# Optimization experiments

Measured on AMD Instinct MI355X. Metric: run time of the kernel, lower is better.

## Reference

```python
import jax, jax.numpy as jnp
import numpy as np

D_MODEL = 384
H = 12
HEAD_DIM = D_MODEL // H
# Faithful to source: scale = (d_model // h) ** (-5)  (likely a typo for -0.5, but we match the code)
SCALE = float(HEAD_DIM) ** (-5.0)


def setup_inputs() -> dict:
    key = jax.random.key(0)
    ks = jax.random.split(key, 6)
    B, N, D = 4096, 49, D_MODEL
    x = jax.random.normal(ks[0], (B, N, D), dtype=jnp.float32)
    mask = jnp.zeros((B, 1, N, N), dtype=jnp.float32)
    s = 1.0 / np.sqrt(D)
    Wq = jax.random.normal(ks[1], (D, D), dtype=jnp.float32) * s
    Wk = jax.random.normal(ks[2], (D, D), dtype=jnp.float32) * s
    Wv = jax.random.normal(ks[3], (D, D), dtype=jnp.float32) * s
    Wp = jax.random.normal(ks[4], (D, D), dtype=jnp.float32) * s
    bq = jnp.zeros((D,), jnp.float32)
    bk = jnp.zeros((D,), jnp.float32)
    bv = jnp.zeros((D,), jnp.float32)
    bp = jnp.zeros((D,), jnp.float32)
    return {"x": x, "mask": mask, "Wq": Wq, "bq": bq, "Wk": Wk, "bk": bk,
            "Wv": Wv, "bv": bv, "Wp": Wp, "bp": bp}


def reference(x, mask, Wq, bq, Wk, bk, Wv, bv, Wp, bp):
    # x: [B, N, D] where B = batch*num_windows, N = window_size**2
    B, N, D = x.shape
    def heads(y):  # [B,N,D] -> [B,H,N,hd]
        return y.reshape(B, N, H, HEAD_DIM).transpose(0, 2, 1, 3)
    q = heads(x @ Wq + bq)
    k = heads(x @ Wk + bk)
    v = heads(x @ Wv + bv)
    scores = jnp.einsum('bhnd,bhmd->bhnm', q, k) * SCALE + mask  # mask broadcasts over heads
    w = jax.nn.softmax(scores, axis=-1)  # dropout=0 -> identity
    o = jnp.einsum('bhnm,bhmd->bhnd', w, v)
    o = o.transpose(0, 2, 1, 3).reshape(B, N, D)
    return o @ Wp + bp
```

## Files before the change

### kernel.cpp

```cpp
#include <hip/hip_runtime.h>


#define NWIN   4096
#define NTOK   49
#define DMODEL 384
#define NH     12
#define HD     32
#define XPITCH 392
#define QPITCH 40
#define VPITCH 72
#define SCALE  2.9802322387695312e-08f
#define NEGBIG -30000.0f

typedef __attribute__((ext_vector_type(8))) short short8;
typedef __attribute__((ext_vector_type(4))) short short4v;
typedef __attribute__((ext_vector_type(4))) float float4v;

__device__ __align__(16) unsigned short g_wT[4 * DMODEL * DMODEL];
__device__ int g_dt;

__device__ __forceinline__ float b2f(unsigned short h) {
  union { unsigned u; float f; } t; t.u = ((unsigned)h) << 16; return t.f;
}
__device__ __forceinline__ unsigned short f2b(float f) {
  union { float f; unsigned u; } t; t.f = f;
  return (unsigned short)((t.u + 0x7fffu + ((t.u >> 16) & 1u)) >> 16);
}

__global__ void detect_dtype(const unsigned short* __restrict__ x) {
  __shared__ int cnt;
  if (threadIdx.x == 0) cnt = 0;
  __syncthreads();
  int local = 0;
  for (int i = threadIdx.x; i < 2048; i += 256) {
    unsigned short h = x[2 * i];
    int e = (h >> 7) & 0xFF;
    if (e >= 0x6A && e <= 0x90) local++;
  }
  atomicAdd(&cnt, local);
  __syncthreads();
  if (threadIdx.x == 0) g_dt = (cnt < 1024) ? 1 : 0;
}

__global__ void prep_weights(const void* __restrict__ Wq,
                             const void* __restrict__ Wk,
                             const void* __restrict__ Wv,
                             const void* __restrict__ Wp) {
  int o = blockIdx.x * 256 + threadIdx.x;
  int e = o & 511;
  int t = o >> 9;
  int l = e >> 3, j = e & 7;
  int c = l & 15, qd = l >> 4;
  int k, col;
  const void* W;
  if (t < 864) {
    int h = t / 72, r = t - h * 72;
    int ks = r / 6, i = r - ks * 6;
    int mat = i >> 1, nt = i & 1;
    W = (mat == 0) ? Wq : (mat == 1) ? Wk : Wv;
    k = ks * 32 + qd * 8 + j;
    col = h * 32 + nt * 16 + c;
  } else {
    int tp = t - 864;
    int wv = tp / 72, r = tp - wv * 72;
    int ks = r / 6, nt = r - ks * 6;
    W = Wp;
    k = ks * 32 + qd * 8 + j;
    col = wv * 96 + nt * 16 + c;
  }
  unsigned short v;
  if (g_dt) v = f2b(((const float*)W)[k * DMODEL + col]);
  else      v = ((const unsigned short*)W)[k * DMODEL + col];
  g_wT[o] = v;
}

#define BAR() do {                                          \
    asm volatile("s_waitcnt lgkmcnt(0)" ::: "memory");      \
    __builtin_amdgcn_s_barrier();                           \
    asm volatile("" ::: "memory");                          \
  } while (0)

__global__ __launch_bounds__(256, 2)
void win_attn(const void* __restrict__ xg_,
              const void* __restrict__ maskg_,
              const void* __restrict__ bqg_,
              const void* __restrict__ bkg_,
              const void* __restrict__ bvg_,
              const void* __restrict__ bpg_,
              void* __restrict__ outg_)
{
  __shared__ __align__(16) short lds[28960];
  const int dt   = g_dt;
  const int win  = blockIdx.x;
  const int tid  = threadIdx.x;
  const int wv   = tid >> 6;
  const int lane = tid & 63;
  const int c    = lane & 15;
  const int qd   = lane >> 4;

  const unsigned short* const wlane = g_wT + lane * 8;

  short8 wb[12];
  #pragma unroll
  for (int t = 0; t < 12; ++t)
    wb[t] = *(const short8*)(wlane + t * 512);

  {
    unsigned* z = (unsigned*)&lds[19208];
    for (int i = tid; i < 4876; i += 256) z[i] = 0u;
  }

  if (dt == 0) {
    const uint4* src = (const uint4*)((const unsigned short*)xg_ + (size_t)win * (NTOK * DMODEL));
    for (int i = tid; i < (NTOK * DMODEL) / 8; i += 256) {
      int row = i / 48, col = i - row * 48;
      *(uint4*)&lds[row * XPITCH + col * 8] = src[i];
    }
  } else {
    const float4* src = (const float4*)((const float*)xg_ + (size_t)win * (NTOK * DMODEL));
    for (int i = tid; i < (NTOK * DMODEL) / 4; i += 256) {
      int row = i / 96, colq = i - row * 96;
      float4 f = src[i];
      short4v p;
      p[0] = (short)f2b(f.x); p[1] = (short)f2b(f.y);
      p[2] = (short)f2b(f.z); p[3] = (short)f2b(f.w);
      *(short4v*)&lds[row * XPITCH + colq * 4] = p;
    }
  }

  short* const sQ = lds + 19208;
  short* const sK = lds + 21168;
  short* const sV = lds + 23128;
  short* const sW = lds + 25432;

  const int arow = (wv * 16 + c < NTOK) ? (wv * 16 + c) : (NTOK - 1);

  float madd[4][4];
  #pragma unroll
  for (int r = 0; r < 4; ++r) {
    int m = wv * 16 + qd * 4 + r;
    #pragma unroll
    for (int nt = 0; nt < 4; ++nt) {
      int n = nt * 16 + c;
      float v;
      if (n < NTOK) {
        if (m < NTOK) {
          size_t off = (size_t)win * (NTOK * NTOK) + m * NTOK + n;
          v = dt ? ((const float*)maskg_)[off] : b2f(((const unsigned short*)maskg_)[off]);
        } else v = 0.f;
      } else v = NEGBIG;
      madd[r][nt] = v;
    }
  }

  BAR();

  short8 xa[12];
  #pragma unroll
  for (int ks = 0; ks < 12; ++ks)
    xa[ks] = *(const short8*)&lds[arow * XPITCH + ks * 32 + qd * 8];

  short* const sO = lds;

  const float4v z4 = {0.f, 0.f, 0.f, 0.f};

  #pragma unroll 1
  for (int h = 0; h < NH; ++h) {
    const unsigned short* const wh = wlane + h * 36864;

    float biasQ[2], biasK[2], biasV[2];
    #pragma unroll
    for (int nt = 0; nt < 2; ++nt) {
      const int col = h * 32 + nt * 16 + c;
      biasQ[nt] = dt ? ((const float*)bqg_)[col] : b2f(((const unsigned short*)bqg_)[col]);
      biasK[nt] = dt ? ((const float*)bkg_)[col] : b2f(((const unsigned short*)bkg_)[col]);
      biasV[nt] = dt ? ((const float*)bvg_)[col] : b2f(((const unsigned short*)bvg_)[col]);
    }

    float4v aQ0 = z4, aQ1 = z4, aK0 = z4, aK1 = z4, aV0 = z4, aV1 = z4;
    #pragma unroll
    for (int ks = 0; ks < 12; ++ks) {
      const int s = (ks & 1) * 6;
      const unsigned short* pf = (ks < 10) ? (wh + ((ks + 2) * 6) * 512)
                                           : (wh + 36864 + ((ks - 10) * 6) * 512);
      aQ0 = __builtin_amdgcn_mfma_f32_16x16x32_bf16(xa[ks], wb[s + 0], aQ0, 0, 0, 0);
      wb[s + 0] = *(const short8*)(pf + 0 * 512);
      aQ1 = __builtin_amdgcn_mfma_f32_16x16x32_bf16(xa[ks], wb[s + 1], aQ1, 0, 0, 0);
      wb[s + 1] = *(const short8*)(pf + 1 * 512);
      aK0 = __builtin_amdgcn_mfma_f32_16x16x32_bf16(xa[ks], wb[s + 2], aK0, 0, 0, 0);
      wb[s + 2] = *(const short8*)(pf + 2 * 512);
      aK1 = __builtin_amdgcn_mfma_f32_16x16x32_bf16(xa[ks], wb[s + 3], aK1, 0, 0, 0);
      wb[s + 3] = *(const short8*)(pf + 3 * 512);
      aV0 = __builtin_amdgcn_mfma_f32_16x16x32_bf16(xa[ks], wb[s + 4], aV0, 0, 0, 0);
      wb[s + 4] = *(const short8*)(pf + 4 * 512);
      aV1 = __builtin_amdgcn_mfma_f32_16x16x32_bf16(xa[ks], wb[s + 5], aV1, 0, 0, 0);
      wb[s + 5] = *(const short8*)(pf + 5 * 512);
    }

    #pragma unroll
    for (int nt = 0; nt < 2; ++nt) {
      const float4v q = nt ? aQ1 : aQ0;
      const float4v k = nt ? aK1 : aK0;
      const float4v v = nt ? aV1 : aV0;
      short4v vp;
      #pragma unroll
      for (int r = 0; r < 4; ++r) {
        const int m = wv * 16 + qd * 4 + r;
        if (m < NTOK) {
          sQ[m * QPITCH + nt * 16 + c] = (short)f2b(q[r] + biasQ[nt]);
          sK[m * QPITCH + nt * 16 + c] = (short)f2b(k[r] + biasK[nt]);
        }
        vp[r] = (short)((m < NTOK) ? f2b(v[r] + biasV[nt]) : (unsigned short)0);
      }
      *(short4v*)&sV[(nt * 16 + c) * VPITCH + wv * 16 + qd * 4] = vp;
    }
    BAR();

    float4v aS[4] = {z4, z4, z4, z4};
    {
      const short8 aq = *(const short8*)&sQ[arow * QPITCH + qd * 8];
      #pragma unroll
      for (int nt = 0; nt < 4; ++nt) {
        int kr = nt * 16 + c; if (kr > NTOK - 1) kr = NTOK - 1;
        const short8 bk8 = *(const short8*)&sK[kr * QPITCH + qd * 8];
        aS[nt] = __builtin_amdgcn_mfma_f32_16x16x32_bf16(aq, bk8, aS[nt], 0, 0, 0);
      }
    }

    #pragma unroll
    for (int r = 0; r < 4; ++r) {
      float s0 = fmaf(aS[0][r], SCALE, madd[r][0]);
      float s1 = fmaf(aS[1][r], SCALE, madd[r][1]);
      float s2 = fmaf(aS[2][r], SCALE, madd[r][2]);
      float s3 = fmaf(aS[3][r], SCALE, madd[r][3]);
      float mx = fmaxf(fmaxf(s0, s1), fmaxf(s2, s3));
      mx = fmaxf(mx, __shfl_xor(mx, 1));
      mx = fmaxf(mx, __shfl_xor(mx, 2));
      mx = fmaxf(mx, __shfl_xor(mx, 4));
      mx = fmaxf(mx, __shfl_xor(mx, 8));
      float e0 = __expf(fminf(s0 - mx, 0.f));
      float e1 = __expf(fminf(s1 - mx, 0.f));
      float e2 = __expf(fminf(s2 - mx, 0.f));
      float e3 = __expf(fminf(s3 - mx, 0.f));
      float sum = e0 + e1 + e2 + e3;
      sum += __shfl_xor(sum, 1);
      sum += __shfl_xor(sum, 2);
      sum += __shfl_xor(sum, 4);
      sum += __shfl_xor(sum, 8);
      float inv = 1.0f / sum;
      int m = wv * 16 + qd * 4 + r;
      if (m < NTOK) {
        sW[m * VPITCH +  0 + c] = (short)f2b(e0 * inv);
        sW[m * VPITCH + 16 + c] = (short)f2b(e1 * inv);
        sW[m * VPITCH + 32 + c] = (short)f2b(e2 * inv);
        sW[m * VPITCH + 48 + c] = (short)f2b(e3 * inv);
      }
    }

    float4v aO0 = z4, aO1 = z4;
    #pragma unroll
    for (int ks = 0; ks < 2; ++ks) {
      const short8 aw = *(const short8*)&sW[arow * VPITCH + ks * 32 + qd * 8];
      const short8 b0 = *(const short8*)&sV[(0 * 16 + c) * VPITCH + ks * 32 + qd * 8];
      const short8 b1 = *(const short8*)&sV[(1 * 16 + c) * VPITCH + ks * 32 + qd * 8];
      aO0 = __builtin_amdgcn_mfma_f32_16x16x32_bf16(aw, b0, aO0, 0, 0, 0);
      aO1 = __builtin_amdgcn_mfma_f32_16x16x32_bf16(aw, b1, aO1, 0, 0, 0);
    }

    #pragma unroll
    for (int r = 0; r < 4; ++r) {
      const int m = wv * 16 + qd * 4 + r;
      if (m < NTOK) {
        sO[m * XPITCH + h * 32 +  0 + c] = (short)f2b(aO0[r]);
        sO[m * XPITCH + h * 32 + 16 + c] = (short)f2b(aO1[r]);
      }
    }
    BAR();
  }

  const unsigned short* const wp = g_wT + 442368 + wv * 36864 + lane * 8;
  #pragma unroll
  for (int t = 0; t < 12; ++t)
    wb[t] = *(const short8*)(wp + t * 512);

  float biasP[6];
  #pragma unroll
  for (int nt = 0; nt < 6; ++nt) {
    const int col = wv * 96 + nt * 16 + c;
    biasP[nt] = dt ? ((const float*)bpg_)[col] : b2f(((const unsigned short*)bpg_)[col]);
  }

  float4v aP[4][6];
  #pragma unroll
  for (int mt = 0; mt < 4; ++mt)
    #pragma unroll
    for (int nt = 0; nt < 6; ++nt) aP[mt][nt] = z4;

  short8 af[2][4];
  #pragma unroll
  for (int mt = 0; mt < 4; ++mt) {
    int row = mt * 16 + c; if (row > NTOK - 1) row = NTOK - 1;
    af[0][mt] = *(const short8*)&sO[row * XPITCH + qd * 8];
  }

  #pragma unroll
  for (int ks = 0; ks < 12; ++ks) {
    const int cs = ks & 1;
    if (ks < 11) {
      #pragma unroll
      for (int mt = 0; mt < 4; ++mt) {
        int row = mt * 16 + c; if (row > NTOK - 1) row = NTOK - 1;
        af[cs ^ 1][mt] = *(const short8*)&sO[row * XPITCH + (ks + 1) * 32 + qd * 8];
      }
    }
    const int s = cs * 6;
    #pragma unroll
    for (int nt = 0; nt < 6; ++nt) {
      aP[0][nt] = __builtin_amdgcn_mfma_f32_16x16x32_bf16(af[cs][0], wb[s + nt], aP[0][nt], 0, 0, 0);
      aP[1][nt] = __builtin_amdgcn_mfma_f32_16x16x32_bf16(af[cs][1], wb[s + nt], aP[1][nt], 0, 0, 0);
      aP[2][nt] = __builtin_amdgcn_mfma_f32_16x16x32_bf16(af[cs][2], wb[s + nt], aP[2][nt], 0, 0, 0);
      aP[3][nt] = __builtin_amdgcn_mfma_f32_16x16x32_bf16(af[cs][3], wb[s + nt], aP[3][nt], 0, 0, 0);
      if (ks < 10) wb[s + nt] = *(const short8*)(wp + ((ks + 2) * 6 + nt) * 512);
    }
  }

  #pragma unroll
  for (int nt = 0; nt < 6; ++nt) {
    const int col = wv * 96 + nt * 16 + c;
    #pragma unroll
    for (int mt = 0; mt < 4; ++mt) {
      #pragma unroll
      for (int r = 0; r < 4; ++r) {
        const int m = mt * 16 + qd * 4 + r;
        if (m < NTOK) {
          const float v = aP[mt][nt][r] + biasP[nt];
          const size_t off = (size_t)win * (NTOK * DMODEL) + m * DMODEL + col;
          if (dt) ((float*)outg_)[off] = v;
          else    ((unsigned short*)outg_)[off] = f2b(v);
        }
      }
    }
  }
}

extern "C" void kernel_launch(void* const* d_in, const int* in_sizes, int n_in,
                              void* d_out, int out_size, void* d_ws, size_t ws_size,
                              hipStream_t stream) {
  const void* x    = d_in[0];
  const void* mask = d_in[1];
  const void* Wq   = d_in[2];
  const void* bq   = d_in[3];
  const void* Wk   = d_in[4];
  const void* bk   = d_in[5];
  const void* Wv   = d_in[6];
  const void* bv   = d_in[7];
  const void* Wp   = d_in[8];
  const void* bp   = d_in[9];

  detect_dtype<<<1, 256, 0, stream>>>((const unsigned short*)x);
  prep_weights<<<(4 * DMODEL * DMODEL) / 256, 256, 0, stream>>>(Wq, Wk, Wv, Wp);
  win_attn<<<NWIN, 256, 0, stream>>>(x, mask, bq, bk, bv, bp, d_out);
}
```

Measured before the change: 1.111 ms.

## Switch attention to 32x32 MFMA tiles with two heads processed concurrently

```diff
diff --git a/kernel.cpp b/kernel.cpp
--- a/kernel.cpp
+++ b/kernel.cpp
@@ -7,14 +7,19 @@
 #define NH     12
 #define HD     32
 #define XPITCH 392
-#define QPITCH 40
-#define VPITCH 72
+#define QP     40
+#define VP     72
 #define SCALE  2.9802322387695312e-08f
 #define NEGBIG -30000.0f
 
-typedef __attribute__((ext_vector_type(8))) short short8;
-typedef __attribute__((ext_vector_type(4))) short short4v;
-typedef __attribute__((ext_vector_type(4))) float float4v;
+#define S_BASE 19208
+#define S_STR  6224
+#define LDS_TOT 31656
+
+typedef __attribute__((ext_vector_type(8)))  short short8;
+typedef __attribute__((ext_vector_type(4)))  short short4v;
+typedef __attribute__((ext_vector_type(4)))  float float4v;
+typedef __attribute__((ext_vector_type(16))) float float16v;
 
 __device__ __align__(16) unsigned short g_wT[4 * DMODEL * DMODEL];
 __device__ int g_dt;
@@ -25,6 +30,11 @@
 __device__ __forceinline__ unsigned short f2b(float f) {
   union { float f; unsigned u; } t; t.f = f;
   return (unsigned short)((t.u + 0x7fffu + ((t.u >> 16) & 1u)) >> 16);
+}
+__device__ __forceinline__ unsigned cvt_pk_bf16(float lo, float hi) {
+  unsigned r;
+  asm("v_cvt_pk_bf16_f32 %0, %1, %2" : "=v"(r) : "v"(lo), "v"(hi));
+  return r;
 }
 
 __global__ void detect_dtype(const unsigned short* __restrict__ x) {
@@ -50,23 +60,21 @@
   int e = o & 511;
   int t = o >> 9;
   int l = e >> 3, j = e & 7;
-  int c = l & 15, qd = l >> 4;
   int k, col;
   const void* W;
   if (t < 864) {
     int h = t / 72, r = t - h * 72;
-    int ks = r / 6, i = r - ks * 6;
-    int mat = i >> 1, nt = i & 1;
+    int ks = r / 3, mat = r - ks * 3;
     W = (mat == 0) ? Wq : (mat == 1) ? Wk : Wv;
-    k = ks * 32 + qd * 8 + j;
-    col = h * 32 + nt * 16 + c;
+    k = ks * 16 + (l >> 5) * 8 + j;
+    col = h * 32 + (l & 31);
   } else {
     int tp = t - 864;
     int wv = tp / 72, r = tp - wv * 72;
     int ks = r / 6, nt = r - ks * 6;
     W = Wp;
-    k = ks * 32 + qd * 8 + j;
-    col = wv * 96 + nt * 16 + c;
+    k = ks * 32 + (l >> 4) * 8 + j;
+    col = wv * 96 + nt * 16 + (l & 15);
   }
   unsigned short v;
   if (g_dt) v = f2b(((const float*)W)[k * DMODEL + col]);
@@ -79,6 +87,9 @@
     __builtin_amdgcn_s_barrier();                           \
     asm volatile("" ::: "memory");                          \
   } while (0)
+
+#define MFMA32(A, B, C) __builtin_amdgcn_mfma_f32_32x32x16_bf16((A), (B), (C), 0, 0, 0)
+#define MFMA16(A, B, C) __builtin_amdgcn_mfma_f32_16x16x32_bf16((A), (B), (C), 0, 0, 0)
 
 __global__ __launch_bounds__(256, 2)
 void win_attn(const void* __restrict__ xg_,
@@ -89,25 +100,31 @@
               const void* __restrict__ bpg_,
               void* __restrict__ outg_)
 {
-  __shared__ __align__(16) short lds[28960];
+  __shared__ __align__(16) short lds[LDS_TOT];
   const int dt   = g_dt;
   const int win  = blockIdx.x;
   const int tid  = threadIdx.x;
   const int wv   = tid >> 6;
   const int lane = tid & 63;
+  const int cl   = lane & 31;
+  const int hi   = lane >> 5;
   const int c    = lane & 15;
   const int qd   = lane >> 4;
-
-  const unsigned short* const wlane = g_wT + lane * 8;
+  const int b    = wv & 1;
+  const int h2   = wv >> 1;
+
+  const unsigned short* const wl = g_wT + lane * 8;
 
   short8 wb[12];
-  #pragma unroll
-  for (int t = 0; t < 12; ++t)
-    wb[t] = *(const short8*)(wlane + t * 512);
-
   {
-    unsigned* z = (unsigned*)&lds[19208];
-    for (int i = tid; i < 4876; i += 256) z[i] = 0u;
+    const unsigned short* w0 = wl + (h2 * 72) * 512;
+    #pragma unroll
+    for (int t = 0; t < 12; ++t) wb[t] = *(const short8*)(w0 + t * 512);
+  }
+
+  {
+    unsigned* z = (unsigned*)&lds[S_BASE];
+    for (int i = tid; i < 6224; i += 256) z[i] = 0u;
   }
 
   if (dt == 0) {
@@ -128,160 +145,187 @@
     }
   }
 
-  short* const sQ = lds + 19208;
-  short* const sK = lds + 21168;
-  short* const sV = lds + 23128;
-  short* const sW = lds + 25432;
-
-  const int arow = (wv * 16 + c < NTOK) ? (wv * 16 + c) : (NTOK - 1);
-
-  float madd[4][4];
-  #pragma unroll
-  for (int r = 0; r < 4; ++r) {
-    int m = wv * 16 + qd * 4 + r;
-    #pragma unroll
-    for (int nt = 0; nt < 4; ++nt) {
-      int n = nt * 16 + c;
-      float v;
-      if (n < NTOK) {
-        if (m < NTOK) {
-          size_t off = (size_t)win * (NTOK * NTOK) + m * NTOK + n;
-          v = dt ? ((const float*)maskg_)[off] : b2f(((const unsigned short*)maskg_)[off]);
-        } else v = 0.f;
-      } else v = NEGBIG;
-      madd[r][nt] = v;
-    }
+  short* const sQh = lds + S_BASE + h2 * S_STR;
+  short* const sKh = sQh + 1960;
+  short* const sVt = sQh + 3920;
+  short* const sO  = lds;
+
+  unsigned maddpk[16];
+  {
+    int qrow = b * 32 + cl; if (qrow > NTOK - 1) qrow = NTOK - 1;
+    const size_t mb = (size_t)win * (NTOK * NTOK) + (size_t)qrow * NTOK;
+    #pragma unroll
+    for (int kt = 0; kt < 2; ++kt)
+      #pragma unroll
+      for (int i = 0; i < 8; ++i) {
+        int k0 = kt * 32 + ((2 * i) & 3) + 8 * ((2 * i) >> 2) + 4 * hi;
+        float m0 = (k0     < NTOK)
+          ? (dt ? ((const float*)maskg_)[mb + k0]     : b2f(((const unsigned short*)maskg_)[mb + k0]))
+          : NEGBIG;
+        float m1 = (k0 + 1 < NTOK)
+          ? (dt ? ((const float*)maskg_)[mb + k0 + 1] : b2f(((const unsigned short*)maskg_)[mb + k0 + 1]))
+          : NEGBIG;
+        maddpk[kt * 8 + i] = cvt_pk_bf16(m0, m1);
+      }
   }
 
   BAR();
 
-  short8 xa[12];
-  #pragma unroll
-  for (int ks = 0; ks < 12; ++ks)
-    xa[ks] = *(const short8*)&lds[arow * XPITCH + ks * 32 + qd * 8];
-
-  short* const sO = lds;
+  short8 xa[24];
+  {
+    const int xrow = b * 32 + cl;
+    const int xr   = (xrow < NTOK) ? xrow : 0;
+    const short8 z8 = {0, 0, 0, 0, 0, 0, 0, 0};
+    #pragma unroll
+    for (int ks = 0; ks < 24; ++ks) {
+      short8 t = *(const short8*)&lds[xr * XPITCH + ks * 16 + hi * 8];
+      xa[ks] = (xrow < NTOK) ? t : z8;
+    }
+  }
 
   const float4v z4 = {0.f, 0.f, 0.f, 0.f};
 
   #pragma unroll 1
-  for (int h = 0; h < NH; ++h) {
-    const unsigned short* const wh = wlane + h * 36864;
-
-    float biasQ[2], biasK[2], biasV[2];
-    #pragma unroll
-    for (int nt = 0; nt < 2; ++nt) {
-      const int col = h * 32 + nt * 16 + c;
-      biasQ[nt] = dt ? ((const float*)bqg_)[col] : b2f(((const unsigned short*)bqg_)[col]);
-      biasK[nt] = dt ? ((const float*)bkg_)[col] : b2f(((const unsigned short*)bkg_)[col]);
-      biasV[nt] = dt ? ((const float*)bvg_)[col] : b2f(((const unsigned short*)bvg_)[col]);
-    }
-
-    float4v aQ0 = z4, aQ1 = z4, aK0 = z4, aK1 = z4, aV0 = z4, aV1 = z4;
-    #pragma unroll
-    for (int ks = 0; ks < 12; ++ks) {
-      const int s = (ks & 1) * 6;
-      const unsigned short* pf = (ks < 10) ? (wh + ((ks + 2) * 6) * 512)
-                                           : (wh + 36864 + ((ks - 10) * 6) * 512);
-      aQ0 = __builtin_amdgcn_mfma_f32_16x16x32_bf16(xa[ks], wb[s + 0], aQ0, 0, 0, 0);
+  for (int p = 0; p < 6; ++p) {
+    const int h = 2 * p + h2;
+    const unsigned short* const wh = wl + h * 72 * 512;
+
+    const int colh = h * 32 + cl;
+    const float biasQ = dt ? ((const float*)bqg_)[colh] : b2f(((const unsigned short*)bqg_)[colh]);
+    const float biasK = dt ? ((const float*)bkg_)[colh] : b2f(((const unsigned short*)bkg_)[colh]);
+    const float biasV = dt ? ((const float*)bvg_)[colh] : b2f(((const unsigned short*)bvg_)[colh]);
+
+    float16v aQ, aK, aV;
+    #pragma unroll
+    for (int i = 0; i < 16; ++i) { aQ[i] = 0.f; aK[i] = 0.f; aV[i] = 0.f; }
+    #pragma unroll
+    for (int ks = 0; ks < 24; ++ks) {
+      const int s = (ks & 3) * 3;
+      const short8 a = xa[ks];
+      aQ = MFMA32(a, wb[s + 0], aQ);
+      aK = MFMA32(a, wb[s + 1], aK);
+      aV = MFMA32(a, wb[s + 2], aV);
+      const unsigned short* pf;
+      if (ks < 20)      pf = wh + ((ks + 4) * 3) * 512;
+      else if (p < 5)   pf = wh + (144 + (ks - 20) * 3) * 512;
+      else              pf = g_wT + 442368 + wv * 36864 + lane * 8 + ((ks - 20) * 3) * 512;
       wb[s + 0] = *(const short8*)(pf + 0 * 512);
-      aQ1 = __builtin_amdgcn_mfma_f32_16x16x32_bf16(xa[ks], wb[s + 1], aQ1, 0, 0, 0);
       wb[s + 1] = *(const short8*)(pf + 1 * 512);
-      aK0 = __builtin_amdgcn_mfma_f32_16x16x32_bf16(xa[ks], wb[s + 2], aK0, 0, 0, 0);
       wb[s + 2] = *(const short8*)(pf + 2 * 512);
-      aK1 = __builtin_amdgcn_mfma_f32_16x16x32_bf16(xa[ks], wb[s + 3], aK1, 0, 0, 0);
-      wb[s + 3] = *(const short8*)(pf + 3 * 512);
-      aV0 = __builtin_amdgcn_mfma_f32_16x16x32_bf16(xa[ks], wb[s + 4], aV0, 0, 0, 0);
-      wb[s + 4] = *(const short8*)(pf + 4 * 512);
-      aV1 = __builtin_amdgcn_mfma_f32_16x16x32_bf16(xa[ks], wb[s + 5], aV1, 0, 0, 0);
-      wb[s + 5] = *(const short8*)(pf + 5 * 512);
-    }
-
-    #pragma unroll
-    for (int nt = 0; nt < 2; ++nt) {
-      const float4v q = nt ? aQ1 : aQ0;
-      const float4v k = nt ? aK1 : aK0;
-      const float4v v = nt ? aV1 : aV0;
-      short4v vp;
+    }
+
+    #pragma unroll
+    for (int i = 0; i < 16; ++i) {
+      const int tok = (i & 3) + 8 * (i >> 2) + 4 * hi + b * 32;
+      if (tok < NTOK) {
+        sQh[tok * QP + cl] = (short)f2b(aQ[i] + biasQ);
+        sKh[tok * QP + cl] = (short)f2b(aK[i] + biasK);
+      }
+    }
+    #pragma unroll
+    for (int i = 0; i < 8; ++i) {
+      const int tok = ((2 * i) & 3) + 8 * ((2 * i) >> 2) + 4 * hi + b * 32;
+      if (tok < NTOK) {
+        float v0 = aV[2 * i] + biasV;
+        float v1 = (tok + 1 < NTOK) ? (aV[2 * i + 1] + biasV) : 0.f;
+        *(unsigned*)&sVt[cl * VP + tok] = cvt_pk_bf16(v0, v1);
+      }
+    }
+    BAR();
+
+    float16v S0, S1;
+    #pragma unroll
+    for (int i = 0; i < 16; ++i) { S0[i] = 0.f; S1[i] = 0.f; }
+    {
+      int qr  = b * 32 + cl; if (qr > NTOK - 1) qr = NTOK - 1;
+      const int kr0 = cl;
+      int kr1 = 32 + cl; if (kr1 > NTOK - 1) kr1 = NTOK - 1;
       #pragma unroll
-      for (int r = 0; r < 4; ++r) {
-        const int m = wv * 16 + qd * 4 + r;
-        if (m < NTOK) {
-          sQ[m * QPITCH + nt * 16 + c] = (short)f2b(q[r] + biasQ[nt]);
-          sK[m * QPITCH + nt * 16 + c] = (short)f2b(k[r] + biasK[nt]);
-        }
-        vp[r] = (short)((m < NTOK) ? f2b(v[r] + biasV[nt]) : (unsigned short)0);
-      }
-      *(short4v*)&sV[(nt * 16 + c) * VPITCH + wv * 16 + qd * 4] = vp;
+      for (int ks = 0; ks < 2; ++ks) {
+        const short8 qf  = *(const short8*)&sQh[qr  * QP + ks * 16 + hi * 8];
+        const short8 kf0 = *(const short8*)&sKh[kr0 * QP + ks * 16 + hi * 8];
+        const short8 kf1 = *(const short8*)&sKh[kr1 * QP + ks * 16 + hi * 8];
+        S0 = MFMA32(kf0, qf, S0);
+        S1 = MFMA32(kf1, qf, S1);
+      }
+    }
+
+    float w32[32];
+    #pragma unroll
+    for (int kt = 0; kt < 2; ++kt)
+      #pragma unroll
+      for (int i = 0; i < 8; ++i) {
+        const unsigned pk = maddpk[kt * 8 + i];
+        const float m0 = __uint_as_float(pk << 16);
+        const float m1 = __uint_as_float(pk & 0xffff0000u);
+        const float sv0 = kt ? S1[2 * i]     : S0[2 * i];
+        const float sv1 = kt ? S1[2 * i + 1] : S0[2 * i + 1];
+        w32[kt * 16 + 2 * i]     = fmaf(sv0, SCALE, m0);
+        w32[kt * 16 + 2 * i + 1] = fmaf(sv1, SCALE, m1);
+      }
+    float t16[16], t8[8], t4[4];
+    #pragma unroll
+    for (int i = 0; i < 16; ++i) t16[i] = fmaxf(w32[2 * i], w32[2 * i + 1]);
+    #pragma unroll
+    for (int i = 0; i < 8; ++i)  t8[i] = fmaxf(t16[2 * i], t16[2 * i + 1]);
+    #pragma unroll
+    for (int i = 0; i < 4; ++i)  t4[i] = fmaxf(t8[2 * i], t8[2 * i + 1]);
+    float mx = fmaxf(fmaxf(t4[0], t4[1]), fmaxf(t4[2], t4[3]));
+    mx = fmaxf(mx, __shfl_xor(mx, 32));
+    #pragma unroll
+    for (int i = 0; i < 32; ++i) w32[i] = __expf(w32[i] - mx);
+    #pragma unroll
+    for (int i = 0; i < 16; ++i) t16[i] = w32[2 * i] + w32[2 * i + 1];
+    #pragma unroll
+    for (int i = 0; i < 8; ++i)  t8[i] = t16[2 * i] + t16[2 * i + 1];
+    #pragma unroll
+    for (int i = 0; i < 4; ++i)  t4[i] = t8[2 * i] + t8[2 * i + 1];
+    float sum = (t4[0] + t4[1]) + (t4[2] + t4[3]);
+    sum += __shfl_xor(sum, 32);
+    const float inv = 1.0f / sum;
+    #pragma unroll
+    for (int i = 0; i < 32; ++i) w32[i] *= inv;
+
+    unsigned pw[16];
+    #pragma unroll
+    for (int i = 0; i < 16; ++i)
+      pw[i] = cvt_pk_bf16(w32[2 * i], w32[2 * i + 1]);
+    short8 pa[4];
+    #pragma unroll
+    for (int ks = 0; ks < 4; ++ks) {
+      const unsigned q0 = pw[ks * 4 + 0], q1 = pw[ks * 4 + 1];
+      const unsigned q2 = pw[ks * 4 + 2], q3 = pw[ks * 4 + 3];
+      const unsigned t0 = hi ? q0 : q2;
+      const unsigned t1 = hi ? q1 : q3;
+      const unsigned x0 = __shfl_xor(t0, 32);
+      const unsigned x1 = __shfl_xor(t1, 32);
+      union { unsigned u[4]; short8 s; } u;
+      u.u[0] = hi ? x0 : q0;
+      u.u[1] = hi ? x1 : q1;
+      u.u[2] = hi ? q2 : x0;
+      u.u[3] = hi ? q3 : x1;
+      pa[ks] = u.s;
+    }
+
+    float16v aO;
+    #pragma unroll
+    for (int i = 0; i < 16; ++i) aO[i] = 0.f;
+    #pragma unroll
+    for (int ks = 0; ks < 4; ++ks) {
+      const short8 bv8 = *(const short8*)&sVt[cl * VP + ks * 16 + hi * 8];
+      aO = MFMA32(pa[ks], bv8, aO);
+    }
+
+    #pragma unroll
+    for (int i = 0; i < 16; ++i) {
+      const int tok = (i & 3) + 8 * (i >> 2) + 4 * hi + b * 32;
+      if (tok < NTOK)
+        sO[tok * XPITCH + h * 32 + cl] = (short)f2b(aO[i]);
     }
     BAR();
-
-    float4v aS[4] = {z4, z4, z4, z4};
-    {
-      const short8 aq = *(const short8*)&sQ[arow * QPITCH + qd * 8];
-      #pragma unroll
-      for (int nt = 0; nt < 4; ++nt) {
-        int kr = nt * 16 + c; if (kr > NTOK - 1) kr = NTOK - 1;
-        const short8 bk8 = *(const short8*)&sK[kr * QPITCH + qd * 8];
-        aS[nt] = __builtin_amdgcn_mfma_f32_16x16x32_bf16(aq, bk8, aS[nt], 0, 0, 0);
-      }
-    }
-
-    #pragma unroll
-    for (int r = 0; r < 4; ++r) {
-      float s0 = fmaf(aS[0][r], SCALE, madd[r][0]);
-      float s1 = fmaf(aS[1][r], SCALE, madd[r][1]);
-      float s2 = fmaf(aS[2][r], SCALE, madd[r][2]);
-      float s3 = fmaf(aS[3][r], SCALE, madd[r][3]);
-      float mx = fmaxf(fmaxf(s0, s1), fmaxf(s2, s3));
-      mx = fmaxf(mx, __shfl_xor(mx, 1));
-      mx = fmaxf(mx, __shfl_xor(mx, 2));
-      mx = fmaxf(mx, __shfl_xor(mx, 4));
-      mx = fmaxf(mx, __shfl_xor(mx, 8));
-      float e0 = __expf(fminf(s0 - mx, 0.f));
-      float e1 = __expf(fminf(s1 - mx, 0.f));
-      float e2 = __expf(fminf(s2 - mx, 0.f));
-      float e3 = __expf(fminf(s3 - mx, 0.f));
-      float sum = e0 + e1 + e2 + e3;
-      sum += __shfl_xor(sum, 1);
-      sum += __shfl_xor(sum, 2);
-      sum += __shfl_xor(sum, 4);
-      sum += __shfl_xor(sum, 8);
-      float inv = 1.0f / sum;
-      int m = wv * 16 + qd * 4 + r;
-      if (m < NTOK) {
-        sW[m * VPITCH +  0 + c] = (short)f2b(e0 * inv);
-        sW[m * VPITCH + 16 + c] = (short)f2b(e1 * inv);
-        sW[m * VPITCH + 32 + c] = (short)f2b(e2 * inv);
-        sW[m * VPITCH + 48 + c] = (short)f2b(e3 * inv);
-      }
-    }
-
-    float4v aO0 = z4, aO1 = z4;
-    #pragma unroll
-    for (int ks = 0; ks < 2; ++ks) {
-      const short8 aw = *(const short8*)&sW[arow * VPITCH + ks * 32 + qd * 8];
-      const short8 b0 = *(const short8*)&sV[(0 * 16 + c) * VPITCH + ks * 32 + qd * 8];
-      const short8 b1 = *(const short8*)&sV[(1 * 16 + c) * VPITCH + ks * 32 + qd * 8];
-      aO0 = __builtin_amdgcn_mfma_f32_16x16x32_bf16(aw, b0, aO0, 0, 0, 0);
-      aO1 = __builtin_amdgcn_mfma_f32_16x16x32_bf16(aw, b1, aO1, 0, 0, 0);
-    }
-
-    #pragma unroll
-    for (int r = 0; r < 4; ++r) {
-      const int m = wv * 16 + qd * 4 + r;
-      if (m < NTOK) {
-        sO[m * XPITCH + h * 32 +  0 + c] = (short)f2b(aO0[r]);
-        sO[m * XPITCH + h * 32 + 16 + c] = (short)f2b(aO1[r]);
-      }
-    }
-    BAR();
   }
 
   const unsigned short* const wp = g_wT + 442368 + wv * 36864 + lane * 8;
-  #pragma unroll
-  for (int t = 0; t < 12; ++t)
-    wb[t] = *(const short8*)(wp + t * 512);
 
   float biasP[6];
   #pragma unroll
@@ -316,10 +360,10 @@
     const int s = cs * 6;
     #pragma unroll
     for (int nt = 0; nt < 6; ++nt) {
-      aP[0][nt] = __builtin_amdgcn_mfma_f32_16x16x32_bf16(af[cs][0], wb[s + nt], aP[0][nt], 0, 0, 0);
-      aP[1][nt] = __builtin_amdgcn_mfma_f32_16x16x32_bf16(af[cs][1], wb[s + nt], aP[1][nt], 0, 0, 0);
-      aP[2][nt] = __builtin_amdgcn_mfma_f32_16x16x32_bf16(af[cs][2], wb[s + nt], aP[2][nt], 0, 0, 0);
-      aP[3][nt] = __builtin_amdgcn_mfma_f32_16x16x32_bf16(af[cs][3], wb[s + nt], aP[3][nt], 0, 0, 0);
+      aP[0][nt] = MFMA16(af[cs][0], wb[s + nt], aP[0][nt]);
+      aP[1][nt] = MFMA16(af[cs][1], wb[s + nt], aP[1][nt]);
+      aP[2][nt] = MFMA16(af[cs][2], wb[s + nt], aP[2][nt]);
+      aP[3][nt] = MFMA16(af[cs][3], wb[s + nt], aP[3][nt]);
       if (ks < 10) wb[s + nt] = *(const short8*)(wp + ((ks + 2) * 6 + nt) * 512);
     }
   }
```

Measured after the change: 1.009 ms. 1.1x faster.
